# Kernel optimization log

Hardware: AMD Instinct MI355X
Metric: run time of the kernel (lower is better)

## Reference

```python
import jax, jax.numpy as jnp
import numpy as np


def setup_inputs() -> dict:
    key = jax.random.key(0)
    k1, k2, k3 = jax.random.split(key, 3)
    B, L, C, H, W = 64, 64, 256, 8, 8
    z = jax.random.normal(k1, (B, L, C, H, W), dtype=jnp.float32)
    # KalmanFilter learned params: gain projection and state-transition (1x1 channel maps)
    W_gain = jax.random.normal(k2, (C, C), dtype=jnp.float32) * (1.0 / np.sqrt(C))
    b_gain = jnp.zeros((C,), dtype=jnp.float32)
    W_pred = jax.random.normal(k3, (C, C), dtype=jnp.float32) * (1.0 / np.sqrt(C))
    b_pred = jnp.zeros((C,), dtype=jnp.float32)
    return {"z": z, "W_gain": W_gain, "b_gain": b_gain, "W_pred": W_pred, "b_pred": b_pred}


def reference(z, W_gain, b_gain, W_pred, b_pred):
    # z: [B, L, C, H, W]
    # calc_gain: per-timestep 1x1 channel projection + sigmoid -> gain in (0,1)
    gain = jax.nn.sigmoid(
        jnp.einsum('oc,blchw->blohw', W_gain, z) + b_gain[:, None, None]
    )  # [B, L, C, H, W]

    def step(prev_z, inputs):
        z_i, k_i = inputs  # each [B, C, H, W]
        # predict on detached previous state (matches previous_z.detach())
        pz = jax.lax.stop_gradient(prev_z)
        z_prime = jnp.einsum('oc,bchw->bohw', W_pred, pz) + b_pred[:, None, None]
        # Kalman update: z_hat = z' + K * (z - z')
        z_hat = z_prime + k_i * (z_i - z_prime)
        return z_hat, None

    init = z[:, 0]  # step 0: z_hat = z[:, 0]
    z_seq = jnp.swapaxes(z[:, 1:], 0, 1)      # [L-1, B, C, H, W]
    k_seq = jnp.swapaxes(gain[:, 1:], 0, 1)   # [L-1, B, C, H, W]
    final, _ = jax.lax.scan(step, init, (z_seq, k_seq))
    return final  # [B, C, H, W]
```

## Files before the change

kernel.cpp:

```cpp
#include <hip/hip_runtime.h>

using f32x4  = __attribute__((ext_vector_type(4))) float;
using u16x8  = __attribute__((ext_vector_type(8))) unsigned short;
using u16x4  = __attribute__((ext_vector_type(4))) unsigned short;
using bf16x8 = __attribute__((ext_vector_type(8))) __bf16;

__device__ __forceinline__ unsigned short f2bf(float f){
  unsigned int u = __builtin_bit_cast(unsigned int, f);
  u += 0x7fffu + ((u >> 16) & 1u);
  return (unsigned short)(u >> 16);
}
__device__ __forceinline__ float bf2f(unsigned short h){
  return __builtin_bit_cast(float, ((unsigned int)h) << 16);
}
__device__ __forceinline__ unsigned short f2h(float f){
  return __builtin_bit_cast(unsigned short, (_Float16)f);
}
__device__ __forceinline__ float h2f(unsigned short h){
  return (float)__builtin_bit_cast(_Float16, h);
}
__device__ __forceinline__ f32x4 mfma_bf16(u16x8 a, u16x8 b, f32x4 c){
  return __builtin_amdgcn_mfma_f32_16x16x32_bf16(
      __builtin_bit_cast(bf16x8, a), __builtin_bit_cast(bf16x8, b), c, 0, 0, 0);
}
__device__ __forceinline__ float fast_sigmoid(float x){
  return __builtin_amdgcn_rcpf(1.0f + __builtin_amdgcn_exp2f(-1.44269504f * x));
}

constexpr int C_  = 256;
constexpr int L_  = 64;
constexpr int CHW = C_ * 64;


#define BAR_LDS() do {                                        \
    asm volatile("s_waitcnt lgkmcnt(0)" ::: "memory");        \
    __builtin_amdgcn_s_barrier();                             \
    asm volatile("" ::: "memory");                            \
  } while (0)


__global__ __launch_bounds__(512, 2)
void kalman_kernel(const float* __restrict__ z,  const float* __restrict__ Wg,
                   const float* __restrict__ bg, const float* __restrict__ Wp,
                   const float* __restrict__ bp, float* __restrict__ out)
{
  __shared__ unsigned short zbuf[4][4096];
  __shared__ unsigned short sbuf[2][4096];
  __shared__ unsigned short kbuf[2][4096];

  const int lx  = (int)blockIdx.x;
  const int xcd = lx & 7;
  const int loc = lx >> 3;
  const int b   = xcd + 8 * (loc >> 2);
  const int q   = loc & 3;

  const int t    = (int)threadIdx.x;
  const int lane = t & 63;
  const int wv   = t >> 6;
  const int role = wv >> 2;
  const int rw   = wv & 3;
  const int m    = lane & 15;
  const int g    = lane >> 4;

  const float* zg = z + (size_t)b * L_ * CHW + q * 16;

  const float* Wsel = (role == 0) ? Wp : Wg;
  const float* bsrc = (role == 0) ? bp : bg;
  u16x8 wf[4][8];
  f32x4 bsel[4];
  #pragma unroll
  for (int mi = 0; mi < 4; ++mi){
    const int mt = rw * 4 + mi;
    const float* src = Wsel + (size_t)(mt * 16 + m) * 256 + g * 8;
    #pragma unroll
    for (int kc = 0; kc < 8; ++kc){
      f32x4 a0 = *(const f32x4*)(src + kc * 32);
      f32x4 a1 = *(const f32x4*)(src + kc * 32 + 4);
      #pragma unroll
      for (int j = 0; j < 4; ++j){
        wf[mi][kc][j]     = f2bf(a0[j]);
        wf[mi][kc][j + 4] = f2bf(a1[j]);
      }
    }
    bsel[mi] = *(const f32x4*)(bsrc + mt * 16 + g * 4);
  }

  const int sp = t & 15;
  const int ss = t >> 4;
  const float* st_src = zg + ss * 8 * 64 + sp;
  const int st_dst = (ss * 16 + sp) * 8;
  const int boff   = g * 128 + m * 8;

  {
    float v0[8], v1[8], v2[8];
    #pragma unroll
    for (int j = 0; j < 8; ++j) v0[j] = st_src[j * 64];
    #pragma unroll
    for (int j = 0; j < 8; ++j) v1[j] = st_src[CHW + j * 64];
    #pragma unroll
    for (int j = 0; j < 8; ++j) v2[j] = st_src[2 * CHW + j * 64];
    u16x8 u0, u1, u2;
    #pragma unroll
    for (int j = 0; j < 8; ++j){ u0[j] = f2bf(v0[j]); u1[j] = f2bf(v1[j]); u2[j] = f2bf(v2[j]); }
    *(u16x8*)(&sbuf[0][st_dst]) = u0;
    *(u16x8*)(&zbuf[1][st_dst]) = u1;
    *(u16x8*)(&zbuf[2][st_dst]) = u2;
  }
  float pf[8];
  const float* pfp = st_src + 3 * (size_t)CHW;
  #pragma unroll
  for (int j = 0; j < 8; ++j) pf[j] = pfp[j * 64];
  pfp += CHW;
  __syncthreads();

  if (role == 1){
    u16x8 zf[8];
    #pragma unroll
    for (int kc = 0; kc < 8; ++kc) zf[kc] = *(const u16x8*)(&zbuf[1][kc * 512 + boff]);
    f32x4 glA[4] = {bsel[0], bsel[1], bsel[2], bsel[3]};
    f32x4 glB[4] = {{0,0,0,0},{0,0,0,0},{0,0,0,0},{0,0,0,0}};
    #pragma unroll
    for (int kc = 0; kc < 4; ++kc)
      #pragma unroll
      for (int mi = 0; mi < 4; ++mi){
        glA[mi] = mfma_bf16(wf[mi][kc],     zf[kc],     glA[mi]);
        glB[mi] = mfma_bf16(wf[mi][kc + 4], zf[kc + 4], glB[mi]);
      }
    #pragma unroll
    for (int mi = 0; mi < 4; ++mi){
      const int ro = (rw * 4 + mi) * 16 + g * 4;
      const int el = ((ro >> 3) * 16 + m) * 8 + (ro & 7);
      u16x4 kk;
      #pragma unroll
      for (int r = 0; r < 4; ++r) kk[r] = f2h(fast_sigmoid(glA[mi][r] + glB[mi][r]));
      *(u16x4*)(&kbuf[1][el]) = kk;
    }
  }
  __syncthreads();

  for (int l = 1; l < 63; ++l){
    if (role == 0){
      const unsigned short* sb  = sbuf[(l - 1) & 1];
      const unsigned short* zbl = zbuf[l & 3];
      const unsigned short* kb  = kbuf[l & 1];
      unsigned short* sbw = sbuf[l & 1];

      u16x8 sf[8];
      #pragma unroll
      for (int kc = 0; kc < 8; ++kc) sf[kc] = *(const u16x8*)(sb + kc * 512 + boff);
      u16x4 zi4[4], k4[4];
      #pragma unroll
      for (int mi = 0; mi < 4; ++mi){
        const int ro = (rw * 4 + mi) * 16 + g * 4;
        const int el = ((ro >> 3) * 16 + m) * 8 + (ro & 7);
        zi4[mi] = *(const u16x4*)(zbl + el);
        k4[mi]  = *(const u16x4*)(kb + el);
      }

      f32x4 zpA[4] = {bsel[0], bsel[1], bsel[2], bsel[3]};
      f32x4 zpB[4] = {{0,0,0,0},{0,0,0,0},{0,0,0,0},{0,0,0,0}};
      __builtin_amdgcn_s_setprio(1);
      #pragma unroll
      for (int kc = 0; kc < 4; ++kc)
        #pragma unroll
        for (int mi = 0; mi < 4; ++mi){
          zpA[mi] = mfma_bf16(wf[mi][kc],     sf[kc],     zpA[mi]);
          zpB[mi] = mfma_bf16(wf[mi][kc + 4], sf[kc + 4], zpB[mi]);
        }
      __builtin_amdgcn_s_setprio(0);

      #pragma unroll
      for (int mi = 0; mi < 4; ++mi){
        const int ro = (rw * 4 + mi) * 16 + g * 4;
        const int el = ((ro >> 3) * 16 + m) * 8 + (ro & 7);
        u16x4 sh;
        #pragma unroll
        for (int r = 0; r < 4; ++r){
          float zpr = zpA[mi][r] + zpB[mi][r];
          float zh  = zpr + h2f(k4[mi][r]) * (bf2f(zi4[mi][r]) - zpr);
          sh[r] = f2bf(zh);
        }
        *(u16x4*)(sbw + el) = sh;
      }

      if (l <= 61){
        u16x8 u;
        #pragma unroll
        for (int j = 0; j < 8; ++j) u[j] = f2bf(pf[j]);
        *(u16x8*)(&zbuf[(l + 2) & 3][st_dst]) = u;
      }
      if (l <= 60){
        #pragma unroll
        for (int j = 0; j < 8; ++j) pf[j] = pfp[j * 64];
        pfp += CHW;
      }
    } else {
      if (l <= 61){
        u16x8 u;
        #pragma unroll
        for (int j = 0; j < 8; ++j) u[j] = f2bf(pf[j]);
        *(u16x8*)(&zbuf[(l + 2) & 3][st_dst]) = u;
      }
      if (l <= 60){
        #pragma unroll
        for (int j = 0; j < 8; ++j) pf[j] = pfp[j * 64];
        pfp += CHW;
      }

      const unsigned short* zb = zbuf[(l + 1) & 3];
      unsigned short* kw = kbuf[(l + 1) & 1];

      u16x8 zf[8];
      #pragma unroll
      for (int kc = 0; kc < 8; ++kc) zf[kc] = *(const u16x8*)(zb + kc * 512 + boff);

      f32x4 glA[4] = {bsel[0], bsel[1], bsel[2], bsel[3]};
      f32x4 glB[4] = {{0,0,0,0},{0,0,0,0},{0,0,0,0},{0,0,0,0}};
      #pragma unroll
      for (int kc = 0; kc < 4; ++kc)
        #pragma unroll
        for (int mi = 0; mi < 4; ++mi){
          glA[mi] = mfma_bf16(wf[mi][kc],     zf[kc],     glA[mi]);
          glB[mi] = mfma_bf16(wf[mi][kc + 4], zf[kc + 4], glB[mi]);
        }

      #pragma unroll
      for (int mi = 0; mi < 4; ++mi){
        const int ro = (rw * 4 + mi) * 16 + g * 4;
        const int el = ((ro >> 3) * 16 + m) * 8 + (ro & 7);
        u16x4 kk;
        #pragma unroll
        for (int r = 0; r < 4; ++r) kk[r] = f2h(fast_sigmoid(glA[mi][r] + glB[mi][r]));
        *(u16x4*)(kw + el) = kk;
      }
    }

    BAR_LDS();
  }

  if (role == 0){
    const unsigned short* sb  = sbuf[0];
    const unsigned short* zbl = zbuf[3];
    const unsigned short* kb  = kbuf[1];

    u16x8 sf[8];
    #pragma unroll
    for (int kc = 0; kc < 8; ++kc) sf[kc] = *(const u16x8*)(sb + kc * 512 + boff);
    u16x4 zi4[4], k4[4];
    #pragma unroll
    for (int mi = 0; mi < 4; ++mi){
      const int ro = (rw * 4 + mi) * 16 + g * 4;
      const int el = ((ro >> 3) * 16 + m) * 8 + (ro & 7);
      zi4[mi] = *(const u16x4*)(zbl + el);
      k4[mi]  = *(const u16x4*)(kb + el);
    }

    f32x4 zpA[4] = {bsel[0], bsel[1], bsel[2], bsel[3]};
    f32x4 zpB[4] = {{0,0,0,0},{0,0,0,0},{0,0,0,0},{0,0,0,0}};
    #pragma unroll
    for (int kc = 0; kc < 4; ++kc)
      #pragma unroll
      for (int mi = 0; mi < 4; ++mi){
        zpA[mi] = mfma_bf16(wf[mi][kc],     sf[kc],     zpA[mi]);
        zpB[mi] = mfma_bf16(wf[mi][kc + 4], sf[kc + 4], zpB[mi]);
      }

    #pragma unroll
    for (int mi = 0; mi < 4; ++mi){
      const int ro = (rw * 4 + mi) * 16 + g * 4;
      float* o = out + ((size_t)b * 256 + ro) * 64 + q * 16 + m;
      #pragma unroll
      for (int r = 0; r < 4; ++r){
        float zpr = zpA[mi][r] + zpB[mi][r];
        o[r * 64] = zpr + h2f(k4[mi][r]) * (bf2f(zi4[mi][r]) - zpr);
      }
    }
  }
}

extern "C" void kernel_launch(void* const* d_in, const int* in_sizes, int n_in,
                              void* d_out, int out_size, void* d_ws, size_t ws_size,
                              hipStream_t stream)
{
  const float* z  = (const float*)d_in[0];
  const float* Wg = (const float*)d_in[1];
  const float* bg = (const float*)d_in[2];
  const float* Wp = (const float*)d_in[3];
  const float* bp = (const float*)d_in[4];
  float* out = (float*)d_out;
  hipLaunchKernelGGL(kalman_kernel, dim3(256), dim3(512), 0, stream,
                     z, Wg, bg, Wp, bp, out);
}
```

Measured before the change: 92.02 us.

## Double workgroup size to 1024 threads, halving per-wave output tiles

Workgroups grow from 512 to 1024 threads, so each of the 8 waves per role owns 2 output row-tiles instead of 4. This halves the serial MFMA chain per wave in the recurrent predict step and frees register-resident weight fragments. Operand fragments are now loaded from LDS inside the k-loop rather than preloaded, and staging uses 4-element instead of 8-element chunks. In exchange, every barrier synchronizes twice as many waves and each wave reads the shared state fragments redundantly, which raises LDS traffic.

Result: no change. 90.51 us (-1.6%).

```diff
diff --git a/kernel.cpp b/kernel.cpp
--- a/kernel.cpp
+++ b/kernel.cpp
@@ -39,7 +39,7 @@
   } while (0)
 
 
-__global__ __launch_bounds__(512, 2)
+__global__ __launch_bounds__(1024, 4)
 void kalman_kernel(const float* __restrict__ z,  const float* __restrict__ Wg,
                    const float* __restrict__ bg, const float* __restrict__ Wp,
                    const float* __restrict__ bp, float* __restrict__ out)
@@ -57,8 +57,8 @@
   const int t    = (int)threadIdx.x;
   const int lane = t & 63;
   const int wv   = t >> 6;
-  const int role = wv >> 2;
-  const int rw   = wv & 3;
+  const int role = wv >> 3;
+  const int rw   = wv & 7;
   const int m    = lane & 15;
   const int g    = lane >> 4;
 
@@ -66,11 +66,11 @@
 
   const float* Wsel = (role == 0) ? Wp : Wg;
   const float* bsrc = (role == 0) ? bp : bg;
-  u16x8 wf[4][8];
-  f32x4 bsel[4];
+  u16x8 wf[2][8];
+  f32x4 bsel[2];
   #pragma unroll
-  for (int mi = 0; mi < 4; ++mi){
-    const int mt = rw * 4 + mi;
+  for (int mi = 0; mi < 2; ++mi){
+    const int mt = rw * 2 + mi;
     const float* src = Wsel + (size_t)(mt * 16 + m) * 256 + g * 8;
     #pragma unroll
     for (int kc = 0; kc < 8; ++kc){
@@ -85,50 +85,46 @@
     bsel[mi] = *(const f32x4*)(bsrc + mt * 16 + g * 4);
   }
 
-  const int sp = t & 15;
-  const int ss = t >> 4;
-  const float* st_src = zg + ss * 8 * 64 + sp;
-  const int st_dst = (ss * 16 + sp) * 8;
+  const int px = t & 15;
+  const int cq = t >> 4;
+  const float* st_src = zg + cq * 4 * 64 + px;
+  const int st_dst = ((cq >> 1) * 16 + px) * 8 + (cq & 1) * 4;
   const int boff   = g * 128 + m * 8;
 
   {
-    float v0[8], v1[8], v2[8];
-    #pragma unroll
-    for (int j = 0; j < 8; ++j) v0[j] = st_src[j * 64];
-    #pragma unroll
-    for (int j = 0; j < 8; ++j) v1[j] = st_src[CHW + j * 64];
-    #pragma unroll
-    for (int j = 0; j < 8; ++j) v2[j] = st_src[2 * CHW + j * 64];
-    u16x8 u0, u1, u2;
-    #pragma unroll
-    for (int j = 0; j < 8; ++j){ u0[j] = f2bf(v0[j]); u1[j] = f2bf(v1[j]); u2[j] = f2bf(v2[j]); }
-    *(u16x8*)(&sbuf[0][st_dst]) = u0;
-    *(u16x8*)(&zbuf[1][st_dst]) = u1;
-    *(u16x8*)(&zbuf[2][st_dst]) = u2;
-  }
-  float pf[8];
+    u16x4 u0, u1, u2;
+    #pragma unroll
+    for (int j = 0; j < 4; ++j){
+      u0[j] = f2bf(st_src[j * 64]);
+      u1[j] = f2bf(st_src[CHW + j * 64]);
+      u2[j] = f2bf(st_src[2 * CHW + j * 64]);
+    }
+    *(u16x4*)(&sbuf[0][st_dst]) = u0;
+    *(u16x4*)(&zbuf[1][st_dst]) = u1;
+    *(u16x4*)(&zbuf[2][st_dst]) = u2;
+  }
+  float pf[4];
   const float* pfp = st_src + 3 * (size_t)CHW;
   #pragma unroll
-  for (int j = 0; j < 8; ++j) pf[j] = pfp[j * 64];
+  for (int j = 0; j < 4; ++j) pf[j] = pfp[j * 64];
   pfp += CHW;
   __syncthreads();
 
   if (role == 1){
-    u16x8 zf[8];
-    #pragma unroll
-    for (int kc = 0; kc < 8; ++kc) zf[kc] = *(const u16x8*)(&zbuf[1][kc * 512 + boff]);
-    f32x4 glA[4] = {bsel[0], bsel[1], bsel[2], bsel[3]};
-    f32x4 glB[4] = {{0,0,0,0},{0,0,0,0},{0,0,0,0},{0,0,0,0}};
-    #pragma unroll
-    for (int kc = 0; kc < 4; ++kc)
-      #pragma unroll
-      for (int mi = 0; mi < 4; ++mi){
-        glA[mi] = mfma_bf16(wf[mi][kc],     zf[kc],     glA[mi]);
-        glB[mi] = mfma_bf16(wf[mi][kc + 4], zf[kc + 4], glB[mi]);
-      }
-    #pragma unroll
-    for (int mi = 0; mi < 4; ++mi){
-      const int ro = (rw * 4 + mi) * 16 + g * 4;
+    f32x4 glA[2] = {bsel[0], bsel[1]};
+    f32x4 glB[2] = {{0,0,0,0},{0,0,0,0}};
+    #pragma unroll
+    for (int kc = 0; kc < 4; ++kc){
+      u16x8 zfa = *(const u16x8*)(&zbuf[1][kc * 512 + boff]);
+      u16x8 zfb = *(const u16x8*)(&zbuf[1][(kc + 4) * 512 + boff]);
+      glA[0] = mfma_bf16(wf[0][kc],     zfa, glA[0]);
+      glA[1] = mfma_bf16(wf[1][kc],     zfa, glA[1]);
+      glB[0] = mfma_bf16(wf[0][kc + 4], zfb, glB[0]);
+      glB[1] = mfma_bf16(wf[1][kc + 4], zfb, glB[1]);
+    }
+    #pragma unroll
+    for (int mi = 0; mi < 2; ++mi){
+      const int ro = (rw * 2 + mi) * 16 + g * 4;
       const int el = ((ro >> 3) * 16 + m) * 8 + (ro & 7);
       u16x4 kk;
       #pragma unroll
@@ -145,33 +141,32 @@
       const unsigned short* kb  = kbuf[l & 1];
       unsigned short* sbw = sbuf[l & 1];
 
-      u16x8 sf[8];
-      #pragma unroll
-      for (int kc = 0; kc < 8; ++kc) sf[kc] = *(const u16x8*)(sb + kc * 512 + boff);
-      u16x4 zi4[4], k4[4];
-      #pragma unroll
-      for (int mi = 0; mi < 4; ++mi){
-        const int ro = (rw * 4 + mi) * 16 + g * 4;
+      u16x4 zi4[2], k4[2];
+      #pragma unroll
+      for (int mi = 0; mi < 2; ++mi){
+        const int ro = (rw * 2 + mi) * 16 + g * 4;
         const int el = ((ro >> 3) * 16 + m) * 8 + (ro & 7);
         zi4[mi] = *(const u16x4*)(zbl + el);
         k4[mi]  = *(const u16x4*)(kb + el);
       }
 
-      f32x4 zpA[4] = {bsel[0], bsel[1], bsel[2], bsel[3]};
-      f32x4 zpB[4] = {{0,0,0,0},{0,0,0,0},{0,0,0,0},{0,0,0,0}};
+      f32x4 zpA[2] = {bsel[0], bsel[1]};
+      f32x4 zpB[2] = {{0,0,0,0},{0,0,0,0}};
       __builtin_amdgcn_s_setprio(1);
       #pragma unroll
-      for (int kc = 0; kc < 4; ++kc)
-        #pragma unroll
-        for (int mi = 0; mi < 4; ++mi){
-          zpA[mi] = mfma_bf16(wf[mi][kc],     sf[kc],     zpA[mi]);
-          zpB[mi] = mfma_bf16(wf[mi][kc + 4], sf[kc + 4], zpB[mi]);
-        }
+      for (int kc = 0; kc < 4; ++kc){
+        u16x8 sfa = *(const u16x8*)(sb + kc * 512 + boff);
+        u16x8 sfb = *(const u16x8*)(sb + (kc + 4) * 512 + boff);
+        zpA[0] = mfma_bf16(wf[0][kc],     sfa, zpA[0]);
+        zpA[1] = mfma_bf16(wf[1][kc],     sfa, zpA[1]);
+        zpB[0] = mfma_bf16(wf[0][kc + 4], sfb, zpB[0]);
+        zpB[1] = mfma_bf16(wf[1][kc + 4], sfb, zpB[1]);
+      }
       __builtin_amdgcn_s_setprio(0);
 
       #pragma unroll
-      for (int mi = 0; mi < 4; ++mi){
-        const int ro = (rw * 4 + mi) * 16 + g * 4;
+      for (int mi = 0; mi < 2; ++mi){
+        const int ro = (rw * 2 + mi) * 16 + g * 4;
         const int el = ((ro >> 3) * 16 + m) * 8 + (ro & 7);
         u16x4 sh;
         #pragma unroll
@@ -184,49 +179,47 @@
       }
 
       if (l <= 61){
-        u16x8 u;
-        #pragma unroll
-        for (int j = 0; j < 8; ++j) u[j] = f2bf(pf[j]);
-        *(u16x8*)(&zbuf[(l + 2) & 3][st_dst]) = u;
+        u16x4 u;
+        #pragma unroll
+        for (int j = 0; j < 4; ++j) u[j] = f2bf(pf[j]);
+        *(u16x4*)(&zbuf[(l + 2) & 3][st_dst]) = u;
       }
       if (l <= 60){
         #pragma unroll
-        for (int j = 0; j < 8; ++j) pf[j] = pfp[j * 64];
+        for (int j = 0; j < 4; ++j) pf[j] = pfp[j * 64];
         pfp += CHW;
       }
     } else {
       if (l <= 61){
-        u16x8 u;
-        #pragma unroll
-        for (int j = 0; j < 8; ++j) u[j] = f2bf(pf[j]);
-        *(u16x8*)(&zbuf[(l + 2) & 3][st_dst]) = u;
+        u16x4 u;
+        #pragma unroll
+        for (int j = 0; j < 4; ++j) u[j] = f2bf(pf[j]);
+        *(u16x4*)(&zbuf[(l + 2) & 3][st_dst]) = u;
       }
       if (l <= 60){
         #pragma unroll
-        for (int j = 0; j < 8; ++j) pf[j] = pfp[j * 64];
+        for (int j = 0; j < 4; ++j) pf[j] = pfp[j * 64];
         pfp += CHW;
       }
 
       const unsigned short* zb = zbuf[(l + 1) & 3];
       unsigned short* kw = kbuf[(l + 1) & 1];
 
-      u16x8 zf[8];
-      #pragma unroll
-      for (int kc = 0; kc < 8; ++kc) zf[kc] = *(const u16x8*)(zb + kc * 512 + boff);
-
-      f32x4 glA[4] = {bsel[0], bsel[1], bsel[2], bsel[3]};
-      f32x4 glB[4] = {{0,0,0,0},{0,0,0,0},{0,0,0,0},{0,0,0,0}};
-      #pragma unroll
-      for (int kc = 0; kc < 4; ++kc)
-        #pragma unroll
-        for (int mi = 0; mi < 4; ++mi){
-          glA[mi] = mfma_bf16(wf[mi][kc],     zf[kc],     glA[mi]);
-          glB[mi] = mfma_bf16(wf[mi][kc + 4], zf[kc + 4], glB[mi]);
-        }
-
-      #pragma unroll
-      for (int mi = 0; mi < 4; ++mi){
-        const int ro = (rw * 4 + mi) * 16 + g * 4;
+      f32x4 glA[2] = {bsel[0], bsel[1]};
+      f32x4 glB[2] = {{0,0,0,0},{0,0,0,0}};
+      #pragma unroll
+      for (int kc = 0; kc < 4; ++kc){
+        u16x8 zfa = *(const u16x8*)(zb + kc * 512 + boff);
+        u16x8 zfb = *(const u16x8*)(zb + (kc + 4) * 512 + boff);
+        glA[0] = mfma_bf16(wf[0][kc],     zfa, glA[0]);
+        glA[1] = mfma_bf16(wf[1][kc],     zfa, glA[1]);
+        glB[0] = mfma_bf16(wf[0][kc + 4], zfb, glB[0]);
+        glB[1] = mfma_bf16(wf[1][kc + 4], zfb, glB[1]);
+      }
+
+      #pragma unroll
+      for (int mi = 0; mi < 2; ++mi){
+        const int ro = (rw * 2 + mi) * 16 + g * 4;
         const int el = ((ro >> 3) * 16 + m) * 8 + (ro & 7);
         u16x4 kk;
         #pragma unroll
@@ -243,31 +236,30 @@
     const unsigned short* zbl = zbuf[3];
     const unsigned short* kb  = kbuf[1];
 
-    u16x8 sf[8];
-    #pragma unroll
-    for (int kc = 0; kc < 8; ++kc) sf[kc] = *(const u16x8*)(sb + kc * 512 + boff);
-    u16x4 zi4[4], k4[4];
-    #pragma unroll
-    for (int mi = 0; mi < 4; ++mi){
-      const int ro = (rw * 4 + mi) * 16 + g * 4;
+    u16x4 zi4[2], k4[2];
+    #pragma unroll
+    for (int mi = 0; mi < 2; ++mi){
+      const int ro = (rw * 2 + mi) * 16 + g * 4;
       const int el = ((ro >> 3) * 16 + m) * 8 + (ro & 7);
       zi4[mi] = *(const u16x4*)(zbl + el);
       k4[mi]  = *(const u16x4*)(kb + el);
     }
 
-    f32x4 zpA[4] = {bsel[0], bsel[1], bsel[2], bsel[3]};
-    f32x4 zpB[4] = {{0,0,0,0},{0,0,0,0},{0,0,0,0},{0,0,0,0}};
-    #pragma unroll
-    for (int kc = 0; kc < 4; ++kc)
-      #pragma unroll
-      for (int mi = 0; mi < 4; ++mi){
-        zpA[mi] = mfma_bf16(wf[mi][kc],     sf[kc],     zpA[mi]);
-        zpB[mi] = mfma_bf16(wf[mi][kc + 4], sf[kc + 4], zpB[mi]);
-      }
-
-    #pragma unroll
-    for (int mi = 0; mi < 4; ++mi){
-      const int ro = (rw * 4 + mi) * 16 + g * 4;
+    f32x4 zpA[2] = {bsel[0], bsel[1]};
+    f32x4 zpB[2] = {{0,0,0,0},{0,0,0,0}};
+    #pragma unroll
+    for (int kc = 0; kc < 4; ++kc){
+      u16x8 sfa = *(const u16x8*)(sb + kc * 512 + boff);
+      u16x8 sfb = *(const u16x8*)(sb + (kc + 4) * 512 + boff);
+      zpA[0] = mfma_bf16(wf[0][kc],     sfa, zpA[0]);
+      zpA[1] = mfma_bf16(wf[1][kc],     sfa, zpA[1]);
+      zpB[0] = mfma_bf16(wf[0][kc + 4], sfb, zpB[0]);
+      zpB[1] = mfma_bf16(wf[1][kc + 4], sfb, zpB[1]);
+    }
+
+    #pragma unroll
+    for (int mi = 0; mi < 2; ++mi){
+      const int ro = (rw * 2 + mi) * 16 + g * 4;
       float* o = out + ((size_t)b * 256 + ro) * 64 + q * 16 + m;
       #pragma unroll
       for (int r = 0; r < 4; ++r){
@@ -288,6 +280,6 @@
   const float* Wp = (const float*)d_in[3];
   const float* bp = (const float*)d_in[4];
   float* out = (float*)d_out;
-  hipLaunchKernelGGL(kalman_kernel, dim3(256), dim3(512), 0, stream,
+  hipLaunchKernelGGL(kalman_kernel, dim3(256), dim3(1024), 0, stream,
                      z, Wg, bg, Wp, bp, out);
 }
```
